# Performance work log

Measured on AMD Instinct MI355X. Metric: run time of the kernel, lower is better.

The kernel has to match this reference:

```python
import jax, jax.numpy as jnp
import numpy as np

THRE = 0.5        # communication threshold
ALPHA = 0.8       # S_e / S_c mix in pattern gate
P_BIAS, P_WEIGHT = 0.1, 0.9
DILATE_K = 3
EPS = 1e-6


def warp_affine(src, M, out_hw):
    """torch F.affine_grid + F.grid_sample (bilinear, zeros padding, align_corners=False).
    src: (B,C,Hs,Ws), M: (B,2,3) normalized affine. Returns (B,C,Ho,Wo)."""
    B, C, Hs, Ws = src.shape
    Ho, Wo = out_hw
    xs = 2.0 * (jnp.arange(Wo, dtype=src.dtype) + 0.5) / Wo - 1.0
    ys = 2.0 * (jnp.arange(Ho, dtype=src.dtype) + 0.5) / Ho - 1.0
    gx, gy = jnp.meshgrid(xs, ys)                                   # (Ho,Wo)
    base = jnp.stack([gx, gy, jnp.ones_like(gx)], axis=-1)          # (Ho,Wo,3)
    g = jnp.einsum('bij,hwj->bhwi', M.astype(src.dtype), base)      # (B,Ho,Wo,2) x,y
    px = ((g[..., 0] + 1.0) * Ws - 1.0) * 0.5
    py = ((g[..., 1] + 1.0) * Hs - 1.0) * 0.5
    x0 = jnp.floor(px); y0 = jnp.floor(py)
    wx1 = px - x0; wx0 = 1.0 - wx1
    wy1 = py - y0; wy0 = 1.0 - wy1
    bidx = jnp.arange(B)[:, None, None]
    def samp(yi, xi):
        yi = yi.astype(jnp.int32); xi = xi.astype(jnp.int32)
        valid = (yi >= 0) & (yi < Hs) & (xi >= 0) & (xi < Ws)
        yc = jnp.clip(yi, 0, Hs - 1); xc = jnp.clip(xi, 0, Ws - 1)
        v = src[bidx, :, yc, xc]                                    # (B,Ho,Wo,C)
        return v * valid[..., None].astype(src.dtype)
    out = (samp(y0, x0) * (wy0 * wx0)[..., None]
         + samp(y0, x0 + 1) * (wy0 * wx1)[..., None]
         + samp(y0 + 1, x0) * (wy1 * wx0)[..., None]
         + samp(y0 + 1, x0 + 1) * (wy1 * wx1)[..., None])
    return jnp.transpose(out, (0, 3, 1, 2))


def masked_quantile(xf, mf, q):
    """torch.quantile(x[mask], q) with linear interpolation. xf:(N,HW) float, mf:(N,HW) bool."""
    xs = jnp.sort(jnp.where(mf, xf, jnp.inf), axis=-1)
    cnt = mf.sum(axis=-1)
    pos = q * jnp.maximum(cnt - 1, 0).astype(xf.dtype)
    lo = jnp.floor(pos).astype(jnp.int32)
    hi = jnp.ceil(pos).astype(jnp.int32)
    frac = pos - lo.astype(xf.dtype)
    vlo = jnp.take_along_axis(xs, lo[:, None], axis=-1)[:, 0]
    vhi = jnp.take_along_axis(xs, hi[:, None], axis=-1)[:, 0]
    val = vlo + frac * (vhi - vlo)
    return jnp.where(cnt > 0, val, jnp.zeros_like(val))


def qnorm01(x, mask, ql=0.2, qh=0.8):
    """_qnorm01_masked: per-image masked quantile normalization to [0,1]."""
    N = x.shape[0]
    xf = x.reshape(N, -1)
    mf = mask.reshape(N, -1) > 0
    lo = masked_quantile(xf, mf, ql)[:, None]
    hi = masked_quantile(xf, mf, qh)[:, None]
    y = jnp.clip((xf - lo) / (hi - lo + EPS), 0.0, 1.0) * mf.astype(x.dtype)
    return y.reshape(x.shape)


def pattern_gate(conf_b, feats_b, vis_b):
    """_build_pattern_gate. Returns P (1,1,H,W) on ego plane."""
    visf = (vis_b > 0).astype(feats_b.dtype)
    energy = jnp.mean(feats_b ** 2, axis=1, keepdims=True)          # (N,1,H,W)
    S_e = qnorm01(energy, vis_b) * visf
    S_c_raw = jnp.max(jax.nn.sigmoid(conf_b), axis=1, keepdims=True)  # A>1 branch
    S_c = qnorm01(S_c_raw, vis_b) * visf
    S_mix = ALPHA * S_e + (1.0 - ALPHA) * S_c
    D_e = qnorm01(1.0 - S_e[0:1], vis_b[0:1])
    D_c = qnorm01(1.0 - S_c[0:1], vis_b[0:1])
    D = (0.7 * D_e + 0.3 * D_c) * visf[0:1]
    m0 = vis_b[0:1].reshape(1, -1) > 0
    q20_e = masked_quantile(S_e[0:1].reshape(1, -1), m0, 0.2)[0]
    q20_c = masked_quantile(S_c[0:1].reshape(1, -1), m0, 0.2)[0]
    Ke = (S_e[0:1] <= q20_e) & (vis_b[0:1] > 0)
    Kc = (S_c[0:1] <= q20_c) & (vis_b[0:1] > 0)
    K_empty = (Ke & Kc).astype(feats_b.dtype)
    Sup_nei = jnp.mean(S_mix[1:] * visf[1:], axis=0, keepdims=True)
    P = D * Sup_nei * (1.0 - K_empty)
    return qnorm01(P, vis_b[0:1]) * visf[0:1]


def dilate(mask, k):
    if k <= 1:
        return mask
    return jax.lax.reduce_window(mask, -jnp.inf, jax.lax.max,
                                 (1, 1, k, k), (1, 1, 1, 1), 'SAME')


def owner_for_batch(feats_b, conf_b, vis_b, base_b):
    """_compute_owner_masks_from_comm for one batch group (N agents), eval mode
    (soft_tau=0 -> hard argmax owner), dual_ratio=0, dilate_k=3, supply='cls'."""
    N = feats_b.shape[0]
    visf = (vis_b > 0).astype(feats_b.dtype)
    S_full = jnp.clip(conf_b, 0.0, 1.0).mean(axis=1, keepdims=True) * visf
    P = pattern_gate(conf_b, feats_b, vis_b)                        # (1,1,H,W)
    S_b = S_full * (P_BIAS + P_WEIGHT * P)                          # broadcast over N
    scores = S_b * visf                                             # (N,1,H,W)
    winner = jnp.argmax(scores, axis=0)                             # (1,H,W)
    onehot = (jnp.arange(N)[:, None, None, None] == winner[None]).astype(feats_b.dtype)
    owner = onehot * (base_b > 0).astype(feats_b.dtype)
    return dilate(owner, DILATE_K)


def forward(x, psm_single, record_len, normalized_affine_matrix):
    B, L = normalized_affine_matrix.shape[:2]
    N = L  # uniform record_len assumed (record_len[b] == L for all b)
    sumN, C, H, W = x.shape
    A = psm_single.shape[1]
    # ego-view warp matrices t_matrix[0, :N] per batch, flattened to (B*N,2,3)
    M = normalized_affine_matrix[:, 0].reshape(B * N, 2, 3)
    ones = jnp.ones((B * N, 1, H, W), x.dtype)
    vis = warp_affine(ones, M, (H, W))          # warp masks
    conf = warp_affine(psm_single, M, (H, W))   # warped confidence maps
    wx = warp_affine(x, M, (H, W))              # warped features
    # Communication: where2comm-style threshold on max-sigmoid confidence; ego always ones
    comm_map = jnp.max(jax.nn.sigmoid(conf), axis=1, keepdims=True)
    comm = (comm_map > THRE).astype(x.dtype)
    comm = comm.reshape(B, N, 1, H, W).at[:, 0].set(1.0)            # (B,N,1,H,W)
    owner = jax.vmap(owner_for_batch)(
        wx.reshape(B, N, C, H, W), conf.reshape(B, N, A, H, W),
        vis.reshape(B, N, 1, H, W), comm)                           # (B,N,1,H,W)
    final = comm * owner
    wxm = wx.reshape(B, N, C, H, W) * final
    # effective rate over non-ego agents
    eff = final[:, 1:].sum(axis=(1, 2, 3, 4)) / ((N - 1) * H * W)
    effective_rate = eff.mean()
    x_out = wxm.max(axis=1)                                         # MaxFusion over agents
    return x_out, effective_rate


def setup_inputs():
    key = jax.random.key(0)
    k1, k2, k3 = jax.random.split(key, 3)
    B, N, C, A, H, W = 4, 5, 64, 2, 128, 256
    x = jax.random.normal(k1, (B * N, C, H, W), jnp.float32)
    psm_single = jax.random.normal(k2, (B * N, A, H, W), jnp.float32)
    record_len = jnp.full((B,), N, jnp.int32)
    eye = jnp.tile(jnp.array([[1.0, 0.0, 0.0], [0.0, 1.0, 0.0]], jnp.float32), (B, N, N, 1, 1))
    mats = eye + 0.05 * jax.random.normal(k3, (B, N, N, 2, 3), jnp.float32)
    return {"x": x, "psm_single": psm_single, "record_len": record_len,
            "normalized_affine_matrix": mats}


def reference(x, psm_single, record_len, normalized_affine_matrix):
    return forward(x, psm_single, record_len, normalized_affine_matrix)
```

## Files before the change

### kernel.cpp

```cpp
#include <hip/hip_runtime.h>

#define W_    256
#define H_    128
#define HW_   32768
#define NB    4
#define NA    5
#define NC    64
#define NIMG  20
#define EPS_  1e-6f

#define TW    32
#define TH    32
#define CAP   3072
#define TRIPS 3

struct Taps { int o00,o01,o10,o11; float w00,w01,w10,w11; };
struct TapsC { int cy0,cy1,cx0,cx1; float w00,w01,w10,w11; };

__device__ inline TapsC make_taps_c(float M0,float M1,float M2,float M3,float M4,float M5,
                                    int h, int w){
  float gx = 2.0f*((float)w+0.5f)/(float)W_ - 1.0f;
  float gy = 2.0f*((float)h+0.5f)/(float)H_ - 1.0f;
  float X = M0*gx + M1*gy + M2;
  float Y = M3*gx + M4*gy + M5;
  float px = ((X+1.0f)*(float)W_ - 1.0f)*0.5f;
  float py = ((Y+1.0f)*(float)H_ - 1.0f)*0.5f;
  float x0f = floorf(px), y0f = floorf(py);
  float wx1 = px-x0f, wy1 = py-y0f;
  float wx0 = 1.0f-wx1, wy0 = 1.0f-wy1;
  int x0=(int)x0f, y0=(int)y0f, x1=x0+1, y1=y0+1;
  bool vx0=(x0>=0)&&(x0<W_), vx1=(x1>=0)&&(x1<W_);
  bool vy0=(y0>=0)&&(y0<H_), vy1=(y1>=0)&&(y1<H_);
  TapsC t;
  t.cx0=min(max(x0,0),W_-1); t.cx1=min(max(x1,0),W_-1);
  t.cy0=min(max(y0,0),H_-1); t.cy1=min(max(y1,0),H_-1);
  t.w00=(vy0&&vx0)?(wy0*wx0):0.f;
  t.w01=(vy0&&vx1)?(wy0*wx1):0.f;
  t.w10=(vy1&&vx0)?(wy1*wx0):0.f;
  t.w11=(vy1&&vx1)?(wy1*wx1):0.f;
  return t;
}

__device__ inline Taps make_taps(const float* __restrict__ M, int h, int w){
  TapsC c = make_taps_c(M[0],M[1],M[2],M[3],M[4],M[5],h,w);
  Taps t;
  t.o00=c.cy0*W_+c.cx0; t.o01=c.cy0*W_+c.cx1; t.o10=c.cy1*W_+c.cx0; t.o11=c.cy1*W_+c.cx1;
  t.w00=c.w00; t.w01=c.w01; t.w10=c.w10; t.w11=c.w11;
  return t;
}

__device__ inline void proj_pt(float M0,float M1,float M2,float M3,float M4,float M5,
                               int h,int w,float&px,float&py){
  float gx = 2.0f*((float)w+0.5f)/(float)W_ - 1.0f;
  float gy = 2.0f*((float)h+0.5f)/(float)H_ - 1.0f;
  float X = M0*gx + M1*gy + M2;
  float Y = M3*gx + M4*gy + M5;
  px = ((X+1.0f)*(float)W_ - 1.0f)*0.5f;
  py = ((Y+1.0f)*(float)H_ - 1.0f)*0.5f;
}

__device__ inline float clip01(float v){ return fminf(fmaxf(v,0.f),1.f); }
__device__ inline float sigmoidf_(float v){
  if (v>=0.f){ float e=expf(-v); return 1.f/(1.f+e); }
  float e=expf(v); return e/(1.f+e);
}
__device__ inline float quantv(int cnt, float q, float vlo, float vhi){
  if (cnt<=0) return 0.f;
  float pos = q*(float)(cnt-1);
  float frac = pos - floorf(pos);
  return vlo + frac*(vhi-vlo);
}
__device__ inline float ge_f(float t, float lo, float hi){
  return clip01((t-lo)/(hi-lo+EPS_));
}

#define SBAR __builtin_amdgcn_sched_barrier(0)

__global__ void k_init(int* counters){ if (threadIdx.x < 1+NIMG) counters[threadIdx.x] = 0; }

__global__ __launch_bounds__(256) void k_warp_stats(
  const float* __restrict__ x, const float* __restrict__ psm, const float* __restrict__ nam,
  float* __restrict__ vis, float* __restrict__ scraw, float* __restrict__ sfull,
  float* __restrict__ energy, int* __restrict__ cntv)
{
  __shared__ __align__(16) float smem[2][CAP];
  int tid = threadIdx.x;
  int tx = blockIdx.x, ty = blockIdx.y, bn = blockIdx.z;
  int b = bn/NA, n = bn - b*NA;
  const float* M = nam + (size_t)(b*NA*NA + n)*6;
  float M0=M[0],M1=M[1],M2=M[2],M3=M[3],M4=M[4],M5=M[5];
  int tw0 = tx*TW, th0 = ty*TH;
  int r  = tid>>3;
  int cb = (tid&7)<<2;
  int h  = th0 + r;
  int w0 = tw0 + cb;

  float pxa,pya,pxb,pyb,pxc,pyc,pxd,pyd;
  proj_pt(M0,M1,M2,M3,M4,M5, th0,      tw0,      pxa,pya);
  proj_pt(M0,M1,M2,M3,M4,M5, th0,      tw0+TW-1, pxb,pyb);
  proj_pt(M0,M1,M2,M3,M4,M5, th0+TH-1, tw0,      pxc,pyc);
  proj_pt(M0,M1,M2,M3,M4,M5, th0+TH-1, tw0+TW-1, pxd,pyd);
  float pxmin=fminf(fminf(pxa,pxb),fminf(pxc,pxd));
  float pxmax=fmaxf(fmaxf(pxa,pxb),fmaxf(pxc,pxd));
  float pymin=fminf(fminf(pya,pyb),fminf(pyc,pyd));
  float pymax=fmaxf(fmaxf(pya,pyb),fmaxf(pyc,pyd));
  int xs = min(max((int)floorf(pxmin)-1, 0), W_-1);
  int xe = min(max((int)floorf(pxmax)+2, 0), W_-1);
  int ys = min(max((int)floorf(pymin)-1, 0), H_-1);
  int ye = min(max((int)floorf(pymax)+2, 0), H_-1);
  int xs4 = xs & ~3;
  int bwid = xe - xs4 + 1, bh = ye - ys + 1;
  int nck = (bwid+3)>>2;
  int bwp = nck<<2;
  int E2 = bh*bwp;
  bool ok = (E2 <= CAP);

  float vvv[4], w00_[4],w01_[4],w10_[4],w11_[4];
  int   gx0[4],gx1[4],gy0c[4],gy1c[4];
  int   rx0[4]; bool vx0f[4];
  #pragma unroll
  for (int k=0;k<4;++k){
    float px,py; proj_pt(M0,M1,M2,M3,M4,M5, h, w0+k, px,py);
    float x0f=floorf(px), y0f=floorf(py);
    float wx1=px-x0f, wx0=1.f-wx1, wy1=py-y0f, wy0=1.f-wy1;
    int x0=(int)x0f, y0=(int)y0f, x1=x0+1, y1=y0+1;
    bool vx0=(x0>=0)&&(x0<W_), vx1=(x1>=0)&&(x1<W_);
    bool vy0=(y0>=0)&&(y0<H_), vy1=(y1>=0)&&(y1<H_);
    float w00=(vy0&&vx0)?(wy0*wx0):0.f;
    float w01=(vy0&&vx1)?(wy0*wx1):0.f;
    float w10=(vy1&&vx0)?(wy1*wx0):0.f;
    float w11=(vy1&&vx1)?(wy1*wx1):0.f;
    w00_[k]=w00; w01_[k]=w01; w10_[k]=w10; w11_[k]=w11;
    vvv[k]=w00+w01+w10+w11;
    gx0[k]=min(max(x0,0),W_-1); gx1[k]=min(max(x1,0),W_-1);
    gy0c[k]=min(max(y0,0),H_-1); gy1c[k]=min(max(y1,0),H_-1);
    rx0[k]=x0; vx0f[k]=vx0;
  }

  size_t idx = (size_t)bn*HW_ + (size_t)h*W_ + w0;
  float acc[4] = {0.f,0.f,0.f,0.f};

  int srcoff[TRIPS]; int ldsbase = (tid>>6)<<6;
  const float* xb0 = x + (size_t)bn*NC*HW_ + (size_t)ys*W_ + xs4;
  if (ok){
    int totq = bh*nck;
    unsigned magic = (unsigned)((0x100000000ULL + (unsigned)nck - 1) / (unsigned)nck);
    int colcap = (W_-4) - xs4;
    #pragma unroll
    for (int k=0;k<TRIPS;++k){
      int qq = min(tid + (k<<8), totq-1);
      int row = (int)__umulhi((unsigned)qq, magic);
      int col = (qq - row*nck)<<2;
      srcoff[k] = row*W_ + min(col, colcap);
    }
  }
  auto issue = [&](int ch, int bsel){
    const float* src = xb0 + (size_t)ch*HW_;
    #pragma unroll
    for (int k=0;k<TRIPS;++k){
      __builtin_amdgcn_global_load_lds(
        (const __attribute__((address_space(1))) void*)(src + srcoff[k]),
        (__attribute__((address_space(3))) void*)&smem[bsel][(ldsbase + (k<<8))<<2],
        16, 0, 0);
    }
  };
  if (ok){ issue(0,0); issue(1,1); }

  {
    const float* p0 = psm + ((size_t)bn*2+0)*HW_;
    const float* p1 = psm + ((size_t)bn*2+1)*HW_;
    int vsum = 0;
    #pragma unroll
    for (int k=0;k<4;++k){
      int o00=gy0c[k]*W_+gx0[k], o01=gy0c[k]*W_+gx1[k];
      int o10=gy1c[k]*W_+gx0[k], o11=gy1c[k]*W_+gx1[k];
      float c0 = w00_[k]*p0[o00]+w01_[k]*p0[o01]+w10_[k]*p0[o10]+w11_[k]*p0[o11];
      float c1 = w00_[k]*p1[o00]+w01_[k]*p1[o01]+w10_[k]*p1[o10]+w11_[k]*p1[o11];
      vis[idx+k]   = vvv[k];
      scraw[idx+k] = fmaxf(sigmoidf_(c0), sigmoidf_(c1));
      sfull[idx+k] = (clip01(c0)+clip01(c1))*0.5f;
      vsum += (vvv[k]>0.f)?1:0;
    }
    #pragma unroll
    for (int off=32;off;off>>=1) vsum += __shfl_down(vsum,off);
    if ((tid&63)==0) atomicAdd(&cntv[bn], vsum);
  }

  if (ok){
    int a0[4],a1[4]; float e0[4],e1[4],f0[4],f1[4];
    #pragma unroll
    for (int k=0;k<4;++k){
      int bc = min(max(rx0[k]-xs4,0), bwp-1);
      a0[k] = (gy0c[k]-ys)*bwp + bc;
      a1[k] = (gy1c[k]-ys)*bwp + bc;
      bool v0 = vx0f[k];
      e0[k] = v0 ? w00_[k] : w01_[k];
      e1[k] = v0 ? w01_[k] : 0.f;
      f0[k] = v0 ? w10_[k] : w11_[k];
      f1[k] = v0 ? w11_[k] : 0.f;
    }
    #pragma unroll 1
    for (int c=0;c<NC;++c){
      asm volatile("s_waitcnt vmcnt(3)" ::: "memory"); SBAR;
      __builtin_amdgcn_s_barrier(); SBAR;
      const float* B = smem[c&1];
      #pragma unroll
      for (int k=0;k<4;++k){
        float r00=B[a0[k]], r01=B[a0[k]+1];
        float r10=B[a1[k]], r11=B[a1[k]+1];
        float v = e0[k]*r00 + e1[k]*r01 + f0[k]*r10 + f1[k]*r11;
        acc[k] += v*v;
      }
      asm volatile("s_waitcnt lgkmcnt(0)" ::: "memory"); SBAR;
      __builtin_amdgcn_s_barrier(); SBAR;
      issue(min(c+2,NC-1), c&1);
    }
    asm volatile("s_waitcnt vmcnt(0)" ::: "memory");
  } else {
    const float* xb = x + (size_t)bn*NC*HW_;
    int go00[4],go01[4],go10[4],go11[4];
    #pragma unroll
    for (int k=0;k<4;++k){
      go00[k]=gy0c[k]*W_+gx0[k]; go01[k]=gy0c[k]*W_+gx1[k];
      go10[k]=gy1c[k]*W_+gx0[k]; go11[k]=gy1c[k]*W_+gx1[k];
    }
    for (int c=0;c<NC;++c){
      const float* pc = xb + (size_t)c*HW_;
      #pragma unroll
      for (int k=0;k<4;++k){
        float v = w00_[k]*pc[go00[k]] + w01_[k]*pc[go01[k]]
                + w10_[k]*pc[go10[k]] + w11_[k]*pc[go11[k]];
        acc[k] += v*v;
      }
    }
  }
  #pragma unroll
  for (int k=0;k<4;++k) energy[idx+k] = acc[k]*(1.0f/64.0f);
}

#define OS_T 1024
__global__ __launch_bounds__(1024) void k_select(
    const float* __restrict__ energy, const float* __restrict__ scraw,
    const float* __restrict__ ppre, const float* __restrict__ vis,
    const int* __restrict__ cnts,
    float* __restrict__ statsE, float* __restrict__ statsC, float* __restrict__ statsP,
    int mode)
{
  __shared__ int hist[16*256];
  __shared__ int cum[256];
  __shared__ unsigned s_pre;
  __shared__ int s_rk;
  int tid = threadIdx.x;
  int t = blockIdx.x;

  const float* d; const float* m; float* stats; int img, r, cnt;
  if (mode==0){
    bool isC = (t>=96); int tt = isC ? t-96 : t;
    if (tt<80){ img=tt>>2; r=tt&3; } else { int j=tt-80; img=(j>>2)*NA; r=4+(j&3); }
    d = (isC?scraw:energy) + (size_t)img*HW_;
    m = vis + (size_t)img*HW_;
    stats = isC?statsC:statsE;
    cnt = cnts[img];
  } else {
    img = t>>2; r = t&3;
    d = ppre + (size_t)img*HW_;
    m = vis + (size_t)(img*NA)*HW_;
    stats = statsP;
    cnt = cnts[img*NA];
  }
  int cm1 = cnt>0 ? cnt-1 : 0;
  float p2 = 0.2f*(float)cm1, p8 = 0.8f*(float)cm1;
  int l2=(int)floorf(p2), h2=(int)ceilf(p2), l8=(int)floorf(p8), h8=(int)ceilf(p8);
  int rank;
  switch(r){
    case 0: rank=l2; break;      case 1: rank=h2; break;
    case 2: rank=l8; break;      case 3: rank=h8; break;
    case 4: rank=cm1-l2; break;  case 5: rank=cm1-h2; break;
    case 6: rank=cm1-l8; break;  default: rank=cm1-h8; break;
  }

  unsigned key[32];
  #pragma unroll
  for (int k=0;k<32;++k){
    int i = tid + (k<<10);
    unsigned u = __float_as_uint(d[i]);
    unsigned kk = (u & 0x80000000u) ? ~u : (u|0x80000000u);
    key[k] = (m[i] > 0.f) ? kk : 0xFFFFFFFFu;
  }

  if (tid==0){ s_pre=0u; s_rk=rank; }
  int slice = tid & 15;
  #pragma unroll
  for (int round=0; round<4; ++round){
    const int shift = 24 - 8*round;
    for (int i=tid;i<16*256;i+=OS_T) hist[i]=0;
    __syncthreads();
    unsigned pre = s_pre;
    if (round==0){
      #pragma unroll
      for (int k=0;k<32;++k)
        atomicAdd(&hist[slice*256 + (key[k]>>24)], 1);
    } else {
      #pragma unroll
      for (int k=0;k<32;++k)
        if ((key[k]>>(shift+8)) == pre)
          atomicAdd(&hist[slice*256 + ((key[k]>>shift)&255u)], 1);
    }
    __syncthreads();
    if (tid<256){
      int tt=0;
      #pragma unroll
      for (int s=0;s<16;++s) tt += hist[s*256+tid];
      cum[tid]=tt;
    }
    __syncthreads();
    if (tid<64){
      int c0=cum[4*tid+0],c1=cum[4*tid+1],c2=cum[4*tid+2],c3=cum[4*tid+3];
      int i0=c0, i1=i0+c1, i2=i1+c2, i3=i2+c3;
      int tot=i3, scan=tot;
      #pragma unroll
      for (int off=1;off<64;off<<=1){ int v=__shfl_up(scan,off); if (tid>=off) scan+=v; }
      int base = scan-tot;
      int rk = s_rk; unsigned pr = s_pre;
      int b0=base, b1=base+i0, b2=base+i1, b3=base+i2, e3=base+i3;
      if      (rk>=b0 && rk<b1){ s_pre=(pr<<8)|(unsigned)(4*tid+0); s_rk=rk-b0; }
      else if (rk>=b1 && rk<b2){ s_pre=(pr<<8)|(unsigned)(4*tid+1); s_rk=rk-b1; }
      else if (rk>=b2 && rk<b3){ s_pre=(pr<<8)|(unsigned)(4*tid+2); s_rk=rk-b2; }
      else if (rk>=b3 && rk<e3){ s_pre=(pr<<8)|(unsigned)(4*tid+3); s_rk=rk-b3; }
    }
    __syncthreads();
  }
  if (tid==0){
    unsigned k = s_pre;
    unsigned u = (k & 0x80000000u) ? (k & 0x7FFFFFFFu) : ~k;
    stats[img*16 + 1 + r] = __uint_as_float(u);
    if (r==0) stats[img*16] = (float)cnt;
  }
}

__global__ void k_params(const float* __restrict__ statsE, const float* __restrict__ statsC,
                         float* __restrict__ params){
  int b = threadIdx.x;
  if (b>=NB) return;
  float* pr = params + b*32;
  for (int n=0;n<NA;++n){
    const float* sE = statsE + (size_t)(b*NA+n)*16;
    const float* sC = statsC + (size_t)(b*NA+n)*16;
    int cE=(int)sE[0], cC=(int)sC[0];
    pr[n]    = quantv(cE,0.2f,sE[1],sE[2]);
    pr[5+n]  = quantv(cE,0.8f,sE[3],sE[4]);
    pr[10+n] = quantv(cC,0.2f,sC[1],sC[2]);
    pr[15+n] = quantv(cC,0.8f,sC[3],sC[4]);
  }
  const float* sE0 = statsE + (size_t)(b*NA)*16;
  const float* sC0 = statsC + (size_t)(b*NA)*16;
  float loe=pr[0], hie=pr[5], loc=pr[10], hic=pr[15];
  float de_lo=0.f,de_hi=0.f,ke=0.f, dc_lo=0.f,dc_hi=0.f,kc=0.f;
  int c0=(int)sE0[0];
  if (c0>0){
    int cm1=c0-1;
    float pos2=0.2f*(float)cm1, pos8=0.8f*(float)cm1;
    float f2=pos2-floorf(pos2), f8=pos8-floorf(pos8);
    float a,bb;
    a=1.f-ge_f(sE0[5],loe,hie); bb=1.f-ge_f(sE0[6],loe,hie); de_lo=a+f2*(bb-a);
    a=1.f-ge_f(sE0[7],loe,hie); bb=1.f-ge_f(sE0[8],loe,hie); de_hi=a+f8*(bb-a);
    a=ge_f(sE0[1],loe,hie);     bb=ge_f(sE0[2],loe,hie);     ke  =a+f2*(bb-a);
  }
  int c0c=(int)sC0[0];
  if (c0c>0){
    int cm1=c0c-1;
    float pos2=0.2f*(float)cm1, pos8=0.8f*(float)cm1;
    float f2=pos2-floorf(pos2), f8=pos8-floorf(pos8);
    float a,bb;
    a=1.f-ge_f(sC0[5],loc,hic); bb=1.f-ge_f(sC0[6],loc,hic); dc_lo=a+f2*(bb-a);
    a=1.f-ge_f(sC0[7],loc,hic); bb=1.f-ge_f(sC0[8],loc,hic); dc_hi=a+f8*(bb-a);
    a=ge_f(sC0[1],loc,hic);     bb=ge_f(sC0[2],loc,hic);     kc  =a+f2*(bb-a);
  }
  pr[20]=de_lo; pr[21]=de_hi; pr[22]=dc_lo; pr[23]=dc_hi; pr[24]=ke; pr[25]=kc;
}

__global__ __launch_bounds__(256) void k_ppre(
  const float* __restrict__ vis, const float* __restrict__ scraw,
  const float* __restrict__ energy, const float* __restrict__ params,
  float* __restrict__ ppre)
{
  int w=threadIdx.x, h=blockIdx.x, b=blockIdx.y;
  int p=h*W_+w;
  const float* pr = params + b*32;
  size_t base = (size_t)b*NA*HW_ + p;
  float se[NA], sc[NA], vf[NA];
  #pragma unroll
  for (int n=0;n<NA;++n){
    float vv = vis[base + (size_t)n*HW_];
    float f = (vv>0.f)?1.f:0.f; vf[n]=f;
    se[n] = clip01((energy[base+(size_t)n*HW_]-pr[n])/(pr[5+n]-pr[n]+EPS_))*f;
    sc[n] = clip01((scraw[base+(size_t)n*HW_]-pr[10+n])/(pr[15+n]-pr[10+n]+EPS_))*f;
  }
  float sup = 0.f;
  #pragma unroll
  for (int n=1;n<NA;++n) sup += (0.8f*se[n]+0.2f*sc[n])*vf[n];
  sup *= 0.25f;
  float de = clip01(((1.f-se[0])-pr[20])/(pr[21]-pr[20]+EPS_))*vf[0];
  float dc = clip01(((1.f-sc[0])-pr[22])/(pr[23]-pr[22]+EPS_))*vf[0];
  float D  = (0.7f*de + 0.3f*dc)*vf[0];
  bool ke = (se[0] <= pr[24]) && (vf[0]>0.f);
  bool kc = (sc[0] <= pr[25]) && (vf[0]>0.f);
  float kem = (ke&&kc)?1.f:0.f;
  ppre[(size_t)b*HW_+p] = D*sup*(1.f-kem);
}

__global__ __launch_bounds__(256) void k_owner(
  const float* __restrict__ vis, const float* __restrict__ scraw,
  const float* __restrict__ sfull, const float* __restrict__ ppre,
  const float* __restrict__ statsP, int* __restrict__ omask)
{
  int w=threadIdx.x,h=blockIdx.x,b=blockIdx.y;
  int p=h*W_+w;
  const float* sP = statsP + b*16;
  int cntP=(int)sP[0];
  float plo = quantv(cntP,0.2f,sP[1],sP[2]);
  float phi = quantv(cntP,0.8f,sP[3],sP[4]);
  size_t base=(size_t)b*NA*HW_+p;
  float vf0 = (vis[base]>0.f)?1.f:0.f;
  float Pf = clip01((ppre[(size_t)b*HW_+p]-plo)/(phi-plo+EPS_))*vf0;
  float gate = 0.1f + 0.9f*Pf;
  int winner=0; float best=-1.f;
  int cbits=0;
  #pragma unroll
  for (int n=0;n<NA;++n){
    float vv = vis[base+(size_t)n*HW_];
    float f=(vv>0.f)?1.f:0.f;
    float s = ((sfull[base+(size_t)n*HW_]*f)*gate)*f;
    if (s>best){best=s;winner=n;}
    bool cm = (n==0) || (scraw[base+(size_t)n*HW_] > 0.5f);
    if (cm) cbits |= 1<<n;
  }
  int ob = ((cbits>>winner)&1) ? (1<<winner) : 0;
  omask[(size_t)b*HW_+p] = ob | (cbits<<8);
}

__global__ __launch_bounds__(256) void k_final(
  const int* __restrict__ omask, int* __restrict__ fmask, int* __restrict__ counter)
{
  int w=threadIdx.x,h=blockIdx.x,b=blockIdx.y;
  int p=h*W_+w;
  const int* om = omask + (size_t)b*HW_;
  int ow=0;
  #pragma unroll
  for (int dy=-1;dy<=1;++dy){
    int y=h+dy; if (y<0||y>=H_) continue;
    #pragma unroll
    for (int dx=-1;dx<=1;++dx){
      int x=w+dx; if (x<0||x>=W_) continue;
      ow |= om[y*W_+x];
    }
  }
  int cbits=(om[p]>>8)&31;
  int fin = ow & cbits & 31;
  fmask[(size_t)b*HW_+p]=fin;
  int cn = __popc(fin & 30);
  for (int off=32;off;off>>=1) cn += __shfl_down(cn,off);
  if ((threadIdx.x&63)==0) atomicAdd(counter, cn);
}

__global__ __launch_bounds__(256, 2) void k_out(
  const float* __restrict__ x, const float* __restrict__ nam,
  const int* __restrict__ fmask, const int* __restrict__ counter,
  float* __restrict__ out, int out_size)
{
  int w=threadIdx.x, h=blockIdx.x, b=blockIdx.y;
  int p=h*W_+w;
  int fin = fmask[(size_t)b*HW_+p] & 31;
  float init = (__popc(fin)<NA) ? 0.f : -__builtin_inff();
  Taps tp[NA];
  #pragma unroll
  for (int n=0;n<NA;++n) tp[n] = make_taps(nam + (size_t)(b*NA*NA+n)*6, h, w);
  #pragma unroll 1
  for (int cb=0; cb<NC/16; ++cb){
    float m[16];
    #pragma unroll
    for (int c=0;c<16;++c) m[c]=init;
    #pragma unroll
    for (int n=0;n<NA;++n){
      if (!((fin>>n)&1)) continue;
      const float* pc = x + ((size_t)(b*NA+n)*NC + cb*16)*HW_;
      float a00[16],a01[16],a10[16],a11[16];
      #pragma unroll
      for (int c=0;c<16;++c){
        a00[c]=pc[tp[n].o00]; a01[c]=pc[tp[n].o01]; a10[c]=pc[tp[n].o10]; a11[c]=pc[tp[n].o11];
        pc += HW_;
      }
      #pragma unroll
      for (int c=0;c<16;++c){
        float v = tp[n].w00*a00[c] + tp[n].w01*a01[c] + tp[n].w10*a10[c] + tp[n].w11*a11[c];
        m[c] = fmaxf(m[c], v);
      }
    }
    #pragma unroll
    for (int c=0;c<16;++c)
      out[(((size_t)b*NC + cb*16 + c)*H_+h)*W_+w] = m[c];
  }
  if (b==0 && h==0 && w==0)
    out[out_size-1] = (float)(*counter) * (1.0f/524288.0f);
}

extern "C" void kernel_launch(void* const* d_in, const int* in_sizes, int n_in,
                              void* d_out, int out_size, void* d_ws, size_t ws_size,
                              hipStream_t stream) {
  (void)in_sizes; (void)n_in; (void)ws_size;
  const float* x   = (const float*)d_in[0];
  const float* psm = (const float*)d_in[1];
  const float* nam = (const float*)d_in[3];
  float* out = (float*)d_out;

  float* ws     = (float*)d_ws;
  float* vis    = ws;
  float* scraw  = vis    + (size_t)NIMG*HW_;
  float* sfull  = scraw  + (size_t)NIMG*HW_;
  float* energy = sfull  + (size_t)NIMG*HW_;
  float* ppre   = energy + (size_t)NIMG*HW_;
  float* statsE = ppre   + (size_t)NB*HW_;
  float* statsC = statsE + NIMG*16;
  float* statsP = statsC + NIMG*16;
  float* params = statsP + NB*16;
  int*   omask  = (int*)(params + NB*32);
  int*   fmask  = omask + (size_t)NB*HW_;
  int*   counter= fmask + (size_t)NB*HW_;
  int*   cntv   = counter + 1;

  hipLaunchKernelGGL(k_init, dim3(1), dim3(64), 0, stream, counter);
  hipLaunchKernelGGL(k_warp_stats, dim3(W_/TW, H_/TH, NIMG), dim3(256), 0, stream,
                     x, psm, nam, vis, scraw, sfull, energy, cntv);
  hipLaunchKernelGGL(k_select, dim3(192), dim3(OS_T), 0, stream,
                     energy, scraw, ppre, vis, cntv, statsE, statsC, statsP, 0);
  hipLaunchKernelGGL(k_params, dim3(1), dim3(64), 0, stream, statsE, statsC, params);
  hipLaunchKernelGGL(k_ppre, dim3(H_,NB), dim3(W_), 0, stream,
                     vis, scraw, energy, params, ppre);
  hipLaunchKernelGGL(k_select, dim3(16), dim3(OS_T), 0, stream,
                     energy, scraw, ppre, vis, cntv, statsE, statsC, statsP, 1);
  hipLaunchKernelGGL(k_owner, dim3(H_,NB), dim3(W_), 0, stream,
                     vis, scraw, sfull, ppre, statsP, omask);
  hipLaunchKernelGGL(k_final, dim3(H_,NB), dim3(W_), 0, stream, omask, fmask, counter);
  hipLaunchKernelGGL(k_out, dim3(H_,NB), dim3(W_), 0, stream,
                     x, nam, fmask, counter, out, out_size);
}
```

Measured before the change: 238.3 us.

## Triple-buffer channel staging with one barrier and halve warp tile height

```diff
diff --git a/kernel.cpp b/kernel.cpp
--- a/kernel.cpp
+++ b/kernel.cpp
@@ -10,44 +10,12 @@
 #define EPS_  1e-6f
 
 #define TW    32
-#define TH    32
-#define CAP   3072
-#define TRIPS 3
+#define TH    16
+#define CAP   2048
+#define TRIPS 2
+#define NBUF  3
 
 struct Taps { int o00,o01,o10,o11; float w00,w01,w10,w11; };
-struct TapsC { int cy0,cy1,cx0,cx1; float w00,w01,w10,w11; };
-
-__device__ inline TapsC make_taps_c(float M0,float M1,float M2,float M3,float M4,float M5,
-                                    int h, int w){
-  float gx = 2.0f*((float)w+0.5f)/(float)W_ - 1.0f;
-  float gy = 2.0f*((float)h+0.5f)/(float)H_ - 1.0f;
-  float X = M0*gx + M1*gy + M2;
-  float Y = M3*gx + M4*gy + M5;
-  float px = ((X+1.0f)*(float)W_ - 1.0f)*0.5f;
-  float py = ((Y+1.0f)*(float)H_ - 1.0f)*0.5f;
-  float x0f = floorf(px), y0f = floorf(py);
-  float wx1 = px-x0f, wy1 = py-y0f;
-  float wx0 = 1.0f-wx1, wy0 = 1.0f-wy1;
-  int x0=(int)x0f, y0=(int)y0f, x1=x0+1, y1=y0+1;
-  bool vx0=(x0>=0)&&(x0<W_), vx1=(x1>=0)&&(x1<W_);
-  bool vy0=(y0>=0)&&(y0<H_), vy1=(y1>=0)&&(y1<H_);
-  TapsC t;
-  t.cx0=min(max(x0,0),W_-1); t.cx1=min(max(x1,0),W_-1);
-  t.cy0=min(max(y0,0),H_-1); t.cy1=min(max(y1,0),H_-1);
-  t.w00=(vy0&&vx0)?(wy0*wx0):0.f;
-  t.w01=(vy0&&vx1)?(wy0*wx1):0.f;
-  t.w10=(vy1&&vx0)?(wy1*wx0):0.f;
-  t.w11=(vy1&&vx1)?(wy1*wx1):0.f;
-  return t;
-}
-
-__device__ inline Taps make_taps(const float* __restrict__ M, int h, int w){
-  TapsC c = make_taps_c(M[0],M[1],M[2],M[3],M[4],M[5],h,w);
-  Taps t;
-  t.o00=c.cy0*W_+c.cx0; t.o01=c.cy0*W_+c.cx1; t.o10=c.cy1*W_+c.cx0; t.o11=c.cy1*W_+c.cx1;
-  t.w00=c.w00; t.w01=c.w01; t.w10=c.w10; t.w11=c.w11;
-  return t;
-}
 
 __device__ inline void proj_pt(float M0,float M1,float M2,float M3,float M4,float M5,
                                int h,int w,float&px,float&py){
@@ -59,6 +27,24 @@
   py = ((Y+1.0f)*(float)H_ - 1.0f)*0.5f;
 }
 
+__device__ inline Taps make_taps(const float* __restrict__ M, int h, int w){
+  float px,py; proj_pt(M[0],M[1],M[2],M[3],M[4],M[5],h,w,px,py);
+  float x0f=floorf(px), y0f=floorf(py);
+  float wx1=px-x0f, wx0=1.f-wx1, wy1=py-y0f, wy0=1.f-wy1;
+  int x0=(int)x0f, y0=(int)y0f, x1=x0+1, y1=y0+1;
+  bool vx0=(x0>=0)&&(x0<W_), vx1=(x1>=0)&&(x1<W_);
+  bool vy0=(y0>=0)&&(y0<H_), vy1=(y1>=0)&&(y1<H_);
+  int cx0=min(max(x0,0),W_-1), cx1=min(max(x1,0),W_-1);
+  int cy0=min(max(y0,0),H_-1), cy1=min(max(y1,0),H_-1);
+  Taps t;
+  t.o00=cy0*W_+cx0; t.o01=cy0*W_+cx1; t.o10=cy1*W_+cx0; t.o11=cy1*W_+cx1;
+  t.w00=(vy0&&vx0)?(wy0*wx0):0.f;
+  t.w01=(vy0&&vx1)?(wy0*wx1):0.f;
+  t.w10=(vy1&&vx0)?(wy1*wx0):0.f;
+  t.w11=(vy1&&vx1)?(wy1*wx1):0.f;
+  return t;
+}
+
 __device__ inline float clip01(float v){ return fminf(fmaxf(v,0.f),1.f); }
 __device__ inline float sigmoidf_(float v){
   if (v>=0.f){ float e=expf(-v); return 1.f/(1.f+e); }
@@ -83,15 +69,15 @@
   float* __restrict__ vis, float* __restrict__ scraw, float* __restrict__ sfull,
   float* __restrict__ energy, int* __restrict__ cntv)
 {
-  __shared__ __align__(16) float smem[2][CAP];
+  __shared__ __align__(16) float smem[NBUF][CAP];
   int tid = threadIdx.x;
   int tx = blockIdx.x, ty = blockIdx.y, bn = blockIdx.z;
   int b = bn/NA, n = bn - b*NA;
   const float* M = nam + (size_t)(b*NA*NA + n)*6;
   float M0=M[0],M1=M[1],M2=M[2],M3=M[3],M4=M[4],M5=M[5];
   int tw0 = tx*TW, th0 = ty*TH;
-  int r  = tid>>3;
-  int cb = (tid&7)<<2;
+  int r  = tid>>4;
+  int cb = (tid&15)<<1;
   int h  = th0 + r;
   int w0 = tw0 + cb;
 
@@ -115,11 +101,11 @@
   int E2 = bh*bwp;
   bool ok = (E2 <= CAP);
 
-  float vvv[4], w00_[4],w01_[4],w10_[4],w11_[4];
-  int   gx0[4],gx1[4],gy0c[4],gy1c[4];
-  int   rx0[4]; bool vx0f[4];
-  #pragma unroll
-  for (int k=0;k<4;++k){
+  float vvv[2], w00_[2],w01_[2],w10_[2],w11_[2];
+  int   gx0[2],gx1[2],gy0c[2],gy1c[2];
+  int   rx0[2]; bool vx0f[2];
+  #pragma unroll
+  for (int k=0;k<2;++k){
     float px,py; proj_pt(M0,M1,M2,M3,M4,M5, h, w0+k, px,py);
     float x0f=floorf(px), y0f=floorf(py);
     float wx1=px-x0f, wx0=1.f-wx1, wy1=py-y0f, wy0=1.f-wy1;
@@ -138,7 +124,7 @@
   }
 
   size_t idx = (size_t)bn*HW_ + (size_t)h*W_ + w0;
-  float acc[4] = {0.f,0.f,0.f,0.f};
+  float acc[2] = {0.f,0.f};
 
   int srcoff[TRIPS]; int ldsbase = (tid>>6)<<6;
   const float* xb0 = x + (size_t)bn*NC*HW_ + (size_t)ys*W_ + xs4;
@@ -171,7 +157,7 @@
     const float* p1 = psm + ((size_t)bn*2+1)*HW_;
     int vsum = 0;
     #pragma unroll
-    for (int k=0;k<4;++k){
+    for (int k=0;k<2;++k){
       int o00=gy0c[k]*W_+gx0[k], o01=gy0c[k]*W_+gx1[k];
       int o10=gy1c[k]*W_+gx0[k], o11=gy1c[k]*W_+gx1[k];
       float c0 = w00_[k]*p0[o00]+w01_[k]*p0[o01]+w10_[k]*p0[o10]+w11_[k]*p0[o11];
@@ -187,9 +173,9 @@
   }
 
   if (ok){
-    int a0[4],a1[4]; float e0[4],e1[4],f0[4],f1[4];
-    #pragma unroll
-    for (int k=0;k<4;++k){
+    int a0[2],a1[2]; float e0[2],e1[2],f0[2],f1[2];
+    #pragma unroll
+    for (int k=0;k<2;++k){
       int bc = min(max(rx0[k]-xs4,0), bwp-1);
       a0[k] = (gy0c[k]-ys)*bwp + bc;
       a1[k] = (gy1c[k]-ys)*bwp + bc;
@@ -201,33 +187,34 @@
     }
     #pragma unroll 1
     for (int c=0;c<NC;++c){
-      asm volatile("s_waitcnt vmcnt(3)" ::: "memory"); SBAR;
+      asm volatile("s_waitcnt vmcnt(2)" ::: "memory"); SBAR;
       __builtin_amdgcn_s_barrier(); SBAR;
-      const float* B = smem[c&1];
-      #pragma unroll
-      for (int k=0;k<4;++k){
+      {
+        int nc2 = c+2 < NC ? c+2 : NC-1;
+        issue(nc2, (c+2)%NBUF);
+      }
+      const float* B = smem[c%NBUF];
+      #pragma unroll
+      for (int k=0;k<2;++k){
         float r00=B[a0[k]], r01=B[a0[k]+1];
         float r10=B[a1[k]], r11=B[a1[k]+1];
         float v = e0[k]*r00 + e1[k]*r01 + f0[k]*r10 + f1[k]*r11;
         acc[k] += v*v;
       }
-      asm volatile("s_waitcnt lgkmcnt(0)" ::: "memory"); SBAR;
-      __builtin_amdgcn_s_barrier(); SBAR;
-      issue(min(c+2,NC-1), c&1);
     }
     asm volatile("s_waitcnt vmcnt(0)" ::: "memory");
   } else {
     const float* xb = x + (size_t)bn*NC*HW_;
-    int go00[4],go01[4],go10[4],go11[4];
-    #pragma unroll
-    for (int k=0;k<4;++k){
+    int go00[2],go01[2],go10[2],go11[2];
+    #pragma unroll
+    for (int k=0;k<2;++k){
       go00[k]=gy0c[k]*W_+gx0[k]; go01[k]=gy0c[k]*W_+gx1[k];
       go10[k]=gy1c[k]*W_+gx0[k]; go11[k]=gy1c[k]*W_+gx1[k];
     }
     for (int c=0;c<NC;++c){
       const float* pc = xb + (size_t)c*HW_;
       #pragma unroll
-      for (int k=0;k<4;++k){
+      for (int k=0;k<2;++k){
         float v = w00_[k]*pc[go00[k]] + w01_[k]*pc[go01[k]]
                 + w10_[k]*pc[go10[k]] + w11_[k]*pc[go11[k]];
         acc[k] += v*v;
@@ -235,7 +222,7 @@
     }
   }
   #pragma unroll
-  for (int k=0;k<4;++k) energy[idx+k] = acc[k]*(1.0f/64.0f);
+  for (int k=0;k<2;++k) energy[idx+k] = acc[k]*(1.0f/64.0f);
 }
 
 #define OS_T 1024
```

New measurement: 249.6 us. +4.7%, slower.
